# Performance work log

Hardware: AMD Instinct MI355X
Metric: run time of the kernel (lower is better)

## Reference

```python
import jax, jax.numpy as jnp
import numpy as np
from jax import lax

B, T, C, DIN, DOUT = 32, 128, 64, 32, 32  # batch, output_channels(seq), input_channels, input_dim, output_dim


def _init_params(key):
    # Mirror torch init: xOps zeros with identity on min(dout,din) diag; hOps = eye.
    # Add small noise so gradients/behavior are non-degenerate.
    k1, k2 = jax.random.split(key)
    eye_x = jnp.zeros((DOUT, DIN), jnp.float32).at[jnp.arange(min(DOUT, DIN)), jnp.arange(min(DOUT, DIN))].set(1.0)
    xOps = jnp.broadcast_to(eye_x, (4, T, C, DOUT, DIN)) + 0.02 * jax.random.normal(k1, (4, T, C, DOUT, DIN), jnp.float32)
    hOps = jnp.broadcast_to(jnp.eye(DOUT, dtype=jnp.float32), (4, T, C, DOUT, DOUT)) + 0.02 * jax.random.normal(k2, (4, T, C, DOUT, DOUT), jnp.float32)
    return xOps, hOps


def setup_inputs() -> dict:
    key = jax.random.key(0)
    kx, kp = jax.random.split(key)
    x = jax.random.normal(kx, (B, T, C, DIN), jnp.float32)
    xOps, hOps = _init_params(kp)
    return {"x": x, "xOps": xOps, "hOps": hOps}


def reference(x, xOps, hOps):
    # x: [B,T,C,Din]; xOps: [4,T,C,Dout,Din]; hOps: [4,T,C,Dout,Dout]
    b, t, c, _ = x.shape
    dout = hOps.shape[-1]
    h0 = jnp.zeros((b, c, dout), x.dtype)
    c0 = jnp.zeros((b, c, dout), x.dtype)

    def step(carry, inp):
        h, cc = carry
        x_t, xop_t, hop_t = inp  # [B,C,Din], [4,C,Dout,Din], [4,C,Dout,Dout]
        # per-channel (grouped) gate pre-activations, 4 gates at once
        X = jnp.einsum('gcij,bcj->gbci', xop_t, x_t) + jnp.einsum('gcij,bcj->gbci', hop_t, h)
        i = jax.nn.sigmoid(X[0])
        f = jax.nn.sigmoid(X[1])
        g = jnp.tanh(X[2])
        o = jax.nn.sigmoid(X[3])
        c_new = f * cc + i * g
        h_new = o * jnp.tanh(c_new)
        return (h_new, c_new), None

    xs = (jnp.swapaxes(x, 0, 1), jnp.swapaxes(xOps, 0, 1), jnp.swapaxes(hOps, 0, 1))
    (h_fin, _), _ = lax.scan(step, (h0, c0), xs)
    return h_fin  # [B,C,Dout]
```

## Files before the change

### kernel.cpp

```cpp
#include <hip/hip_runtime.h>
#include <stdint.h>

#define T_STEPS 128
#define C_CH    64
#define D_IN    32
#define D_OUT   32

#define RS 72

using frag_ab = __attribute__((ext_vector_type(8))) short;
using frag_cd = __attribute__((ext_vector_type(4))) float;

__device__ __forceinline__ void lds_barrier() {
  asm volatile("s_waitcnt lgkmcnt(0)\n\ts_barrier" ::: "memory");
}

__device__ __forceinline__ uint32_t pack_hi16(uint32_t u0, uint32_t u1) {
  return __builtin_amdgcn_perm(u1, u0, 0x07060302u);
}

__device__ __forceinline__ float fast_sigmoid(float v) {
  return __builtin_amdgcn_rcpf(1.0f + __expf(-v));
}
__device__ __forceinline__ float fast_tanh(float v) {
  return fmaf(2.0f, __builtin_amdgcn_rcpf(1.0f + __expf(-2.0f * v)), -1.0f);
}

__global__ void __launch_bounds__(256)
lstm_kernel(const float* __restrict__ x, const float* __restrict__ xOps,
            const float* __restrict__ hOps, float* __restrict__ out) {
  __shared__ short Ahi[128 * RS];
  __shared__ short Alo[128 * RS];
  __shared__ short Bhi[16 * RS];
  __shared__ short Blo[16 * RS];
  __shared__ float exch[4 * 32 * 9];

  const int tid = threadIdx.x;
  const int c   = blockIdx.x & 63;
  const int q   = blockIdx.x >> 6;

  for (int idx = tid; idx < (16 * RS) / 2; idx += 256) {
    ((uint32_t*)Bhi)[idx] = 0u;
    ((uint32_t*)Blo)[idx] = 0u;
  }

  const float* wptr[8];
  int wlds[8];
#pragma unroll
  for (int it = 0; it < 8; ++it) {
    int f  = (it * 256 + tid) * 4;
    int fh = f & 4095;
    int g  = fh >> 10;
    int i  = (fh >> 5) & 31;
    int j  = fh & 31;
    const float* base = (f < 4096) ? xOps : hOps;
    wptr[it] = base + (size_t)g * (T_STEPS * C_CH * 1024) + (size_t)c * 1024 + i * 32 + j;
    int k = j + ((f < 4096) ? 0 : 32);
    wlds[it] = (g * 32 + i) * RS + k;
  }

  const float* xptr = x;
  int xlds = 0;
  if (tid < 128) {
    int bl = tid >> 4;
    int kp = (tid & 15) * 2;
    int bg = q * 8 + bl;
    xptr = x + (size_t)bg * (T_STEPS * C_CH * D_IN) + (size_t)c * D_IN + kp;
    xlds = bl * RS + kp;
  }

  const int wave   = tid >> 6;
  const int lane   = tid & 63;
  const int frag_n = lane & 15;
  const int quad   = lane >> 4;

  const int eb = tid >> 5;
  const int ei = tid & 31;

  float4 wv[8];
#pragma unroll
  for (int it = 0; it < 8; ++it) wv[it] = *(const float4*)wptr[it];
  float2 xv = make_float2(0.f, 0.f);
  if (tid < 128) xv = *(const float2*)xptr;

  lds_barrier();

  float c_state = 0.0f;

#pragma unroll 1
  for (int t = 0; t < T_STEPS; ++t) {
#pragma unroll
    for (int it = 0; it < 8; ++it) {
      float4 v = wv[it];
      uint32_t u0 = __float_as_uint(v.x), u1 = __float_as_uint(v.y);
      uint32_t u2 = __float_as_uint(v.z), u3 = __float_as_uint(v.w);
      float r0 = v.x - __uint_as_float(u0 & 0xFFFF0000u);
      float r1 = v.y - __uint_as_float(u1 & 0xFFFF0000u);
      float r2 = v.z - __uint_as_float(u2 & 0xFFFF0000u);
      float r3 = v.w - __uint_as_float(u3 & 0xFFFF0000u);
      int s = wlds[it];
      *(uint2*)&Ahi[s] = make_uint2(pack_hi16(u0, u1), pack_hi16(u2, u3));
      *(uint2*)&Alo[s] = make_uint2(pack_hi16(__float_as_uint(r0), __float_as_uint(r1)),
                                    pack_hi16(__float_as_uint(r2), __float_as_uint(r3)));
    }
    if (tid < 128) {
      uint32_t u0 = __float_as_uint(xv.x), u1 = __float_as_uint(xv.y);
      float r0 = xv.x - __uint_as_float(u0 & 0xFFFF0000u);
      float r1 = xv.y - __uint_as_float(u1 & 0xFFFF0000u);
      *(uint32_t*)&Bhi[xlds] = pack_hi16(u0, u1);
      *(uint32_t*)&Blo[xlds] = pack_hi16(__float_as_uint(r0), __float_as_uint(r1));
    }

    if (t + 1 < T_STEPS) {
#pragma unroll
      for (int it = 0; it < 8; ++it)
        wv[it] = *(const float4*)(wptr[it] + (size_t)(t + 1) * (C_CH * 1024));
      if (tid < 128) xv = *(const float2*)(xptr + (size_t)(t + 1) * (C_CH * D_IN));
    }

    lds_barrier();

    frag_cd acc0 = {0.f, 0.f, 0.f, 0.f};
    frag_cd acc1 = {0.f, 0.f, 0.f, 0.f};
#pragma unroll
    for (int kt = 0; kt < 2; ++kt) {
      const int kk = kt * 32 + quad * 8;
      frag_ab bh = *(const frag_ab*)&Bhi[frag_n * RS + kk];
      frag_ab bl = *(const frag_ab*)&Blo[frag_n * RS + kk];
      {
        int m = wave * 32 + frag_n;
        frag_ab ah = *(const frag_ab*)&Ahi[m * RS + kk];
        frag_ab al = *(const frag_ab*)&Alo[m * RS + kk];
        acc0 = __builtin_amdgcn_mfma_f32_16x16x32_bf16(ah, bh, acc0, 0, 0, 0);
        acc0 = __builtin_amdgcn_mfma_f32_16x16x32_bf16(ah, bl, acc0, 0, 0, 0);
        acc0 = __builtin_amdgcn_mfma_f32_16x16x32_bf16(al, bh, acc0, 0, 0, 0);
      }
      {
        int m = wave * 32 + 16 + frag_n;
        frag_ab ah = *(const frag_ab*)&Ahi[m * RS + kk];
        frag_ab al = *(const frag_ab*)&Alo[m * RS + kk];
        acc1 = __builtin_amdgcn_mfma_f32_16x16x32_bf16(ah, bh, acc1, 0, 0, 0);
        acc1 = __builtin_amdgcn_mfma_f32_16x16x32_bf16(ah, bl, acc1, 0, 0, 0);
        acc1 = __builtin_amdgcn_mfma_f32_16x16x32_bf16(al, bh, acc1, 0, 0, 0);
      }
    }

    if (frag_n < 8) {
#pragma unroll
      for (int r = 0; r < 4; ++r) {
        exch[(wave * 32 + quad * 4 + r) * 9 + frag_n]      = acc0[r];
        exch[(wave * 32 + 16 + quad * 4 + r) * 9 + frag_n] = acc1[r];
      }
    }

    lds_barrier();

    {
      float X0 = exch[(0 * 32 + ei) * 9 + eb];
      float X1 = exch[(1 * 32 + ei) * 9 + eb];
      float X2 = exch[(2 * 32 + ei) * 9 + eb];
      float X3 = exch[(3 * 32 + ei) * 9 + eb];
      float ig = fast_sigmoid(X0);
      float fg = fast_sigmoid(X1);
      float gg = fast_tanh(X2);
      float og = fast_sigmoid(X3);
      c_state = fg * c_state + ig * gg;
      float hval = og * fast_tanh(c_state);
      if (t == T_STEPS - 1) {
        out[((size_t)(q * 8 + eb) * C_CH + c) * D_OUT + ei] = hval;
      } else {
        uint32_t u  = __float_as_uint(hval);
        float    r  = hval - __uint_as_float(u & 0xFFFF0000u);
        uint32_t ru = __float_as_uint(r);
        uint32_t pu  = __shfl_xor(u, 1, 64);
        uint32_t pru = __shfl_xor(ru, 1, 64);
        if ((ei & 1) == 0) {
          *(uint32_t*)&Bhi[eb * RS + 32 + ei] = pack_hi16(u, pu);
          *(uint32_t*)&Blo[eb * RS + 32 + ei] = pack_hi16(ru, pru);
        }
      }
    }
  }
}

extern "C" void kernel_launch(void* const* d_in, const int* in_sizes, int n_in,
                              void* d_out, int out_size, void* d_ws, size_t ws_size,
                              hipStream_t stream) {
  const float* x    = (const float*)d_in[0];
  const float* xOps = (const float*)d_in[1];
  const float* hOps = (const float*)d_in[2];
  lstm_kernel<<<dim3(256), dim3(256), 0, stream>>>(x, xOps, hOps, (float*)d_out);
}
```

Before: 359.2 us.

## Process all batches per channel in one block with double-buffered weight prefetch

Changes the decomposition from 256 blocks (channel × batch-quarter of 8 rows) to 64 blocks of 512 threads, each handling all 32 batch rows for one channel. Each step's weights are now read once per channel instead of four times, and loads are double-buffered two steps ahead to hide global latency. The cost is only 64 blocks on a GPU with many more CUs, so parallelism drops, and each block does more MFMA and gate work per step on the serial critical path.

```diff
diff --git a/kernel.cpp b/kernel.cpp
--- a/kernel.cpp
+++ b/kernel.cpp
@@ -7,6 +7,7 @@
 #define D_OUT   32
 
 #define RS 72
+#define ES 34
 
 using frag_ab = __attribute__((ext_vector_type(8))) short;
 using frag_cd = __attribute__((ext_vector_type(4))) float;
@@ -26,71 +27,62 @@
   return fmaf(2.0f, __builtin_amdgcn_rcpf(1.0f + __expf(-2.0f * v)), -1.0f);
 }
 
-__global__ void __launch_bounds__(256)
+__global__ void __launch_bounds__(512, 2)
 lstm_kernel(const float* __restrict__ x, const float* __restrict__ xOps,
             const float* __restrict__ hOps, float* __restrict__ out) {
   __shared__ short Ahi[128 * RS];
   __shared__ short Alo[128 * RS];
-  __shared__ short Bhi[16 * RS];
-  __shared__ short Blo[16 * RS];
-  __shared__ float exch[4 * 32 * 9];
+  __shared__ short Bhi[32 * RS];
+  __shared__ short Blo[32 * RS];
+  __shared__ float exch[4 * 32 * ES];
 
   const int tid = threadIdx.x;
-  const int c   = blockIdx.x & 63;
-  const int q   = blockIdx.x >> 6;
+  const int c   = blockIdx.x;
 
-  for (int idx = tid; idx < (16 * RS) / 2; idx += 256) {
+  for (int idx = tid; idx < (32 * RS) / 2; idx += 512) {
     ((uint32_t*)Bhi)[idx] = 0u;
     ((uint32_t*)Blo)[idx] = 0u;
   }
 
-  const float* wptr[8];
-  int wlds[8];
+  const float* wptr[4];
+  int wlds[4];
 #pragma unroll
-  for (int it = 0; it < 8; ++it) {
-    int f  = (it * 256 + tid) * 4;
+  for (int it = 0; it < 4; ++it) {
+    int f  = (it * 512 + tid) * 4;
     int fh = f & 4095;
     int g  = fh >> 10;
     int i  = (fh >> 5) & 31;
     int j  = fh & 31;
     const float* base = (f < 4096) ? xOps : hOps;
     wptr[it] = base + (size_t)g * (T_STEPS * C_CH * 1024) + (size_t)c * 1024 + i * 32 + j;
-    int k = j + ((f < 4096) ? 0 : 32);
-    wlds[it] = (g * 32 + i) * RS + k;
+    wlds[it] = (g * 32 + i) * RS + j + ((f < 4096) ? 0 : 32);
   }
 
-  const float* xptr = x;
-  int xlds = 0;
-  if (tid < 128) {
-    int bl = tid >> 4;
-    int kp = (tid & 15) * 2;
-    int bg = q * 8 + bl;
-    xptr = x + (size_t)bg * (T_STEPS * C_CH * D_IN) + (size_t)c * D_IN + kp;
-    xlds = bl * RS + kp;
-  }
+  const int bl = tid >> 4;
+  const int kp = (tid & 15) * 2;
+  const float* xptr = x + (size_t)bl * (T_STEPS * C_CH * D_IN) + (size_t)c * D_IN + kp;
+  const int xlds = bl * RS + kp;
 
-  const int wave   = tid >> 6;
-  const int lane   = tid & 63;
-  const int frag_n = lane & 15;
-  const int quad   = lane >> 4;
+  const int wave = tid >> 6;
+  const int lane = tid & 63;
+  const int g    = wave & 3;
+  const int bh   = wave >> 2;
+  const int fn   = lane & 15;
+  const int quad = lane >> 4;
 
-  const int eb = tid >> 5;
-  const int ei = tid & 31;
+  const int ei  = tid & 31;
+  const int eb0 = tid >> 5;
 
-  float4 wv[8];
+  auto load = [&](float4 wv[4], float2& xv, int t) {
 #pragma unroll
-  for (int it = 0; it < 8; ++it) wv[it] = *(const float4*)wptr[it];
-  float2 xv = make_float2(0.f, 0.f);
-  if (tid < 128) xv = *(const float2*)xptr;
+    for (int it = 0; it < 4; ++it)
+      wv[it] = *(const float4*)(wptr[it] + (size_t)t * (C_CH * 1024));
+    xv = *(const float2*)(xptr + (size_t)t * (C_CH * D_IN));
+  };
 
-  lds_barrier();
-
-  float c_state = 0.0f;
-
-#pragma unroll 1
-  for (int t = 0; t < T_STEPS; ++t) {
+  auto stage = [&](const float4 wv[4], float2 xv) {
 #pragma unroll
-    for (int it = 0; it < 8; ++it) {
+    for (int it = 0; it < 4; ++it) {
       float4 v = wv[it];
       uint32_t u0 = __float_as_uint(v.x), u1 = __float_as_uint(v.y);
       uint32_t u2 = __float_as_uint(v.z), u3 = __float_as_uint(v.w);
@@ -103,19 +95,30 @@
       *(uint2*)&Alo[s] = make_uint2(pack_hi16(__float_as_uint(r0), __float_as_uint(r1)),
                                     pack_hi16(__float_as_uint(r2), __float_as_uint(r3)));
     }
-    if (tid < 128) {
-      uint32_t u0 = __float_as_uint(xv.x), u1 = __float_as_uint(xv.y);
-      float r0 = xv.x - __uint_as_float(u0 & 0xFFFF0000u);
-      float r1 = xv.y - __uint_as_float(u1 & 0xFFFF0000u);
-      *(uint32_t*)&Bhi[xlds] = pack_hi16(u0, u1);
-      *(uint32_t*)&Blo[xlds] = pack_hi16(__float_as_uint(r0), __float_as_uint(r1));
-    }
+    uint32_t u0 = __float_as_uint(xv.x), u1 = __float_as_uint(xv.y);
+    float r0 = xv.x - __uint_as_float(u0 & 0xFFFF0000u);
+    float r1 = xv.y - __uint_as_float(u1 & 0xFFFF0000u);
+    *(uint32_t*)&Bhi[xlds] = pack_hi16(u0, u1);
+    *(uint32_t*)&Blo[xlds] = pack_hi16(__float_as_uint(r0), __float_as_uint(r1));
+  };
 
-    if (t + 1 < T_STEPS) {
-#pragma unroll
-      for (int it = 0; it < 8; ++it)
-        wv[it] = *(const float4*)(wptr[it] + (size_t)(t + 1) * (C_CH * 1024));
-      if (tid < 128) xv = *(const float2*)(xptr + (size_t)(t + 1) * (C_CH * D_IN));
+  float4 wv0[4], wv1[4];
+  float2 xv0, xv1;
+  load(wv0, xv0, 0);
+  load(wv1, xv1, 1);
+
+  lds_barrier();
+
+  float cs0 = 0.0f, cs1 = 0.0f;
+
+#pragma unroll 1
+  for (int t = 0; t < T_STEPS; ++t) {
+    if ((t & 1) == 0) {
+      stage(wv0, xv0);
+      if (t + 2 < T_STEPS) load(wv0, xv0, t + 2);
+    } else {
+      stage(wv1, xv1);
+      if (t + 2 < T_STEPS) load(wv1, xv1, t + 2);
     }
 
     lds_barrier();
@@ -125,58 +128,59 @@
 #pragma unroll
     for (int kt = 0; kt < 2; ++kt) {
       const int kk = kt * 32 + quad * 8;
-      frag_ab bh = *(const frag_ab*)&Bhi[frag_n * RS + kk];
-      frag_ab bl = *(const frag_ab*)&Blo[frag_n * RS + kk];
+      frag_ab bhf = *(const frag_ab*)&Bhi[(bh * 16 + fn) * RS + kk];
+      frag_ab blf = *(const frag_ab*)&Blo[(bh * 16 + fn) * RS + kk];
       {
-        int m = wave * 32 + frag_n;
+        int m = g * 32 + fn;
         frag_ab ah = *(const frag_ab*)&Ahi[m * RS + kk];
         frag_ab al = *(const frag_ab*)&Alo[m * RS + kk];
-        acc0 = __builtin_amdgcn_mfma_f32_16x16x32_bf16(ah, bh, acc0, 0, 0, 0);
-        acc0 = __builtin_amdgcn_mfma_f32_16x16x32_bf16(ah, bl, acc0, 0, 0, 0);
-        acc0 = __builtin_amdgcn_mfma_f32_16x16x32_bf16(al, bh, acc0, 0, 0, 0);
+        acc0 = __builtin_amdgcn_mfma_f32_16x16x32_bf16(ah, bhf, acc0, 0, 0, 0);
+        acc0 = __builtin_amdgcn_mfma_f32_16x16x32_bf16(ah, blf, acc0, 0, 0, 0);
+        acc0 = __builtin_amdgcn_mfma_f32_16x16x32_bf16(al, bhf, acc0, 0, 0, 0);
       }
       {
-        int m = wave * 32 + 16 + frag_n;
+        int m = g * 32 + 16 + fn;
         frag_ab ah = *(const frag_ab*)&Ahi[m * RS + kk];
         frag_ab al = *(const frag_ab*)&Alo[m * RS + kk];
-        acc1 = __builtin_amdgcn_mfma_f32_16x16x32_bf16(ah, bh, acc1, 0, 0, 0);
-        acc1 = __builtin_amdgcn_mfma_f32_16x16x32_bf16(ah, bl, acc1, 0, 0, 0);
-        acc1 = __builtin_amdgcn_mfma_f32_16x16x32_bf16(al, bh, acc1, 0, 0, 0);
+        acc1 = __builtin_amdgcn_mfma_f32_16x16x32_bf16(ah, bhf, acc1, 0, 0, 0);
+        acc1 = __builtin_amdgcn_mfma_f32_16x16x32_bf16(ah, blf, acc1, 0, 0, 0);
+        acc1 = __builtin_amdgcn_mfma_f32_16x16x32_bf16(al, bhf, acc1, 0, 0, 0);
       }
     }
 
-    if (frag_n < 8) {
 #pragma unroll
-      for (int r = 0; r < 4; ++r) {
-        exch[(wave * 32 + quad * 4 + r) * 9 + frag_n]      = acc0[r];
-        exch[(wave * 32 + 16 + quad * 4 + r) * 9 + frag_n] = acc1[r];
-      }
+    for (int r = 0; r < 4; ++r) {
+      exch[(g * 32 + quad * 4 + r) * ES + bh * 16 + fn]      = acc0[r];
+      exch[(g * 32 + 16 + quad * 4 + r) * ES + bh * 16 + fn] = acc1[r];
     }
 
     lds_barrier();
 
-    {
-      float X0 = exch[(0 * 32 + ei) * 9 + eb];
-      float X1 = exch[(1 * 32 + ei) * 9 + eb];
-      float X2 = exch[(2 * 32 + ei) * 9 + eb];
-      float X3 = exch[(3 * 32 + ei) * 9 + eb];
+#pragma unroll
+    for (int half = 0; half < 2; ++half) {
+      const int b = eb0 + half * 16;
+      float X0 = exch[(0 * 32 + ei) * ES + b];
+      float X1 = exch[(1 * 32 + ei) * ES + b];
+      float X2 = exch[(2 * 32 + ei) * ES + b];
+      float X3 = exch[(3 * 32 + ei) * ES + b];
       float ig = fast_sigmoid(X0);
       float fg = fast_sigmoid(X1);
       float gg = fast_tanh(X2);
       float og = fast_sigmoid(X3);
-      c_state = fg * c_state + ig * gg;
-      float hval = og * fast_tanh(c_state);
+      float& cs = half ? cs1 : cs0;
+      cs = fg * cs + ig * gg;
+      float hval = og * fast_tanh(cs);
       if (t == T_STEPS - 1) {
-        out[((size_t)(q * 8 + eb) * C_CH + c) * D_OUT + ei] = hval;
+        out[((size_t)b * C_CH + c) * D_OUT + ei] = hval;
       } else {
-        uint32_t u  = __float_as_uint(hval);
-        float    r  = hval - __uint_as_float(u & 0xFFFF0000u);
-        uint32_t ru = __float_as_uint(r);
+        uint32_t u   = __float_as_uint(hval);
+        float    rr  = hval - __uint_as_float(u & 0xFFFF0000u);
+        uint32_t ru  = __float_as_uint(rr);
         uint32_t pu  = __shfl_xor(u, 1, 64);
         uint32_t pru = __shfl_xor(ru, 1, 64);
         if ((ei & 1) == 0) {
-          *(uint32_t*)&Bhi[eb * RS + 32 + ei] = pack_hi16(u, pu);
-          *(uint32_t*)&Blo[eb * RS + 32 + ei] = pack_hi16(ru, pru);
+          *(uint32_t*)&Bhi[b * RS + 32 + ei] = pack_hi16(u, pu);
+          *(uint32_t*)&Blo[b * RS + 32 + ei] = pack_hi16(ru, pru);
         }
       }
     }
@@ -189,5 +193,5 @@
   const float* x    = (const float*)d_in[0];
   const float* xOps = (const float*)d_in[1];
   const float* hOps = (const float*)d_in[2];
-  lstm_kernel<<<dim3(256), dim3(256), 0, stream>>>(x, xOps, hOps, (float*)d_out);
+  lstm_kernel<<<dim3(C_CH), dim3(512), 0, stream>>>(x, xOps, hOps, (float*)d_out);
 }
```

New measurement: 496.7 us. +38.3%, slower.

## Replace split-bf16 MFMA gate GEMM with register-resident fp32 FMA and shuffle reduction

Applied to the files above, without the earlier changes.

Each block no longer splits weights into hi/lo bf16 halves, stages them in LDS and runs three MFMAs per tile. Each thread now keeps its slice of the weight rows in registers and does fp32 FMAs against the shared x/h vector. Partial sums across the four k-quarters are reduced with lane shuffles. Weight loads are double-buffered two steps ahead, using two register sets and an unrolled pair of steps. This removes the per-step bf16 conversion and the large LDS writes, and keeps exact fp32 accuracy, at the cost of more VALU FMAs and higher register pressure.

```diff
diff --git a/kernel.cpp b/kernel.cpp
--- a/kernel.cpp
+++ b/kernel.cpp
@@ -3,20 +3,11 @@
 
 #define T_STEPS 128
 #define C_CH    64
-#define D_IN    32
-#define D_OUT   32
-
-#define RS 72
-
-using frag_ab = __attribute__((ext_vector_type(8))) short;
-using frag_cd = __attribute__((ext_vector_type(4))) float;
+#define SROW    72
+#define EROW    10
 
 __device__ __forceinline__ void lds_barrier() {
   asm volatile("s_waitcnt lgkmcnt(0)\n\ts_barrier" ::: "memory");
-}
-
-__device__ __forceinline__ uint32_t pack_hi16(uint32_t u0, uint32_t u1) {
-  return __builtin_amdgcn_perm(u1, u0, 0x07060302u);
 }
 
 __device__ __forceinline__ float fast_sigmoid(float v) {
@@ -26,160 +17,116 @@
   return fmaf(2.0f, __builtin_amdgcn_rcpf(1.0f + __expf(-2.0f * v)), -1.0f);
 }
 
-__global__ void __launch_bounds__(256)
+__global__ void __launch_bounds__(256, 1)
 lstm_kernel(const float* __restrict__ x, const float* __restrict__ xOps,
             const float* __restrict__ hOps, float* __restrict__ out) {
-  __shared__ short Ahi[128 * RS];
-  __shared__ short Alo[128 * RS];
-  __shared__ short Bhi[16 * RS];
-  __shared__ short Blo[16 * RS];
-  __shared__ float exch[4 * 32 * 9];
+  __shared__ float S[8 * SROW];
+  __shared__ float exch[128 * EROW];
 
   const int tid = threadIdx.x;
   const int c   = blockIdx.x & 63;
   const int q   = blockIdx.x >> 6;
 
-  for (int idx = tid; idx < (16 * RS) / 2; idx += 256) {
-    ((uint32_t*)Bhi)[idx] = 0u;
-    ((uint32_t*)Blo)[idx] = 0u;
-  }
+  const int kq = tid & 3;
+  const int iq = (tid >> 2) & 15;
+  const int g  = tid >> 6;
 
-  const float* wptr[8];
-  int wlds[8];
-#pragma unroll
-  for (int it = 0; it < 8; ++it) {
-    int f  = (it * 256 + tid) * 4;
-    int fh = f & 4095;
-    int g  = fh >> 10;
-    int i  = (fh >> 5) & 31;
-    int j  = fh & 31;
-    const float* base = (f < 4096) ? xOps : hOps;
-    wptr[it] = base + (size_t)g * (T_STEPS * C_CH * 1024) + (size_t)c * 1024 + i * 32 + j;
-    int k = j + ((f < 4096) ? 0 : 32);
-    wlds[it] = (g * 32 + i) * RS + k;
-  }
+  S[(tid >> 5) * SROW + 32 + (tid & 31)] = 0.0f;
 
-  const float* xptr = x;
-  int xlds = 0;
-  if (tid < 128) {
-    int bl = tid >> 4;
-    int kp = (tid & 15) * 2;
-    int bg = q * 8 + bl;
-    xptr = x + (size_t)bg * (T_STEPS * C_CH * D_IN) + (size_t)c * D_IN + kp;
-    xlds = bl * RS + kp;
-  }
+  const float* wbase = (kq < 2) ? xOps : hOps;
+  const int    jo    = (kq & 1) * 16;
+  const float* wp0 = wbase + ((size_t)g * T_STEPS * C_CH + c) * 1024 + iq * 32 + jo;
+  const float* wp1 = wp0 + 512;
+  const size_t WT  = (size_t)C_CH * 1024;
 
-  const int wave   = tid >> 6;
-  const int lane   = tid & 63;
-  const int frag_n = lane & 15;
-  const int quad   = lane >> 4;
+  const int bx = tid >> 3, jx = (tid & 7) * 4;
+  const float* xp = x + (size_t)(q * 8 + bx) * (T_STEPS * C_CH * 32) + c * 32 + jx;
+  const size_t XT = (size_t)C_CH * 32;
 
   const int eb = tid >> 5;
   const int ei = tid & 31;
 
-  float4 wv[8];
+  auto loadw = [&](float4 w0[4], float4 w1[4], int t) {
 #pragma unroll
-  for (int it = 0; it < 8; ++it) wv[it] = *(const float4*)wptr[it];
-  float2 xv = make_float2(0.f, 0.f);
-  if (tid < 128) xv = *(const float2*)xptr;
+    for (int it = 0; it < 4; ++it) {
+      w0[it] = *(const float4*)(wp0 + (size_t)t * WT + it * 4);
+      w1[it] = *(const float4*)(wp1 + (size_t)t * WT + it * 4);
+    }
+  };
 
-  lds_barrier();
+  float4 wa0[4], wa1[4], wb0[4], wb1[4];
+  float4 xa = make_float4(0.f, 0.f, 0.f, 0.f), xb = xa;
+  loadw(wa0, wa1, 0);
+  loadw(wb0, wb1, 1);
+  if (tid < 64) { xa = *(const float4*)xp; xb = *(const float4*)(xp + XT); }
 
-  float c_state = 0.0f;
+  float cs = 0.0f;
 
-#pragma unroll 1
-  for (int t = 0; t < T_STEPS; ++t) {
-#pragma unroll
-    for (int it = 0; it < 8; ++it) {
-      float4 v = wv[it];
-      uint32_t u0 = __float_as_uint(v.x), u1 = __float_as_uint(v.y);
-      uint32_t u2 = __float_as_uint(v.z), u3 = __float_as_uint(v.w);
-      float r0 = v.x - __uint_as_float(u0 & 0xFFFF0000u);
-      float r1 = v.y - __uint_as_float(u1 & 0xFFFF0000u);
-      float r2 = v.z - __uint_as_float(u2 & 0xFFFF0000u);
-      float r3 = v.w - __uint_as_float(u3 & 0xFFFF0000u);
-      int s = wlds[it];
-      *(uint2*)&Ahi[s] = make_uint2(pack_hi16(u0, u1), pack_hi16(u2, u3));
-      *(uint2*)&Alo[s] = make_uint2(pack_hi16(__float_as_uint(r0), __float_as_uint(r1)),
-                                    pack_hi16(__float_as_uint(r2), __float_as_uint(r3)));
-    }
-    if (tid < 128) {
-      uint32_t u0 = __float_as_uint(xv.x), u1 = __float_as_uint(xv.y);
-      float r0 = xv.x - __uint_as_float(u0 & 0xFFFF0000u);
-      float r1 = xv.y - __uint_as_float(u1 & 0xFFFF0000u);
-      *(uint32_t*)&Bhi[xlds] = pack_hi16(u0, u1);
-      *(uint32_t*)&Blo[xlds] = pack_hi16(__float_as_uint(r0), __float_as_uint(r1));
-    }
-
-    if (t + 1 < T_STEPS) {
-#pragma unroll
-      for (int it = 0; it < 8; ++it)
-        wv[it] = *(const float4*)(wptr[it] + (size_t)(t + 1) * (C_CH * 1024));
-      if (tid < 128) xv = *(const float2*)(xptr + (size_t)(t + 1) * (C_CH * D_IN));
-    }
-
+  auto step = [&](int t, float4 w0[4], float4 w1[4], float4& xv) {
+    if (tid < 64) *(float4*)&S[bx * SROW + jx] = xv;
     lds_barrier();
 
-    frag_cd acc0 = {0.f, 0.f, 0.f, 0.f};
-    frag_cd acc1 = {0.f, 0.f, 0.f, 0.f};
+    float acc0[8], acc1[8];
 #pragma unroll
-    for (int kt = 0; kt < 2; ++kt) {
-      const int kk = kt * 32 + quad * 8;
-      frag_ab bh = *(const frag_ab*)&Bhi[frag_n * RS + kk];
-      frag_ab bl = *(const frag_ab*)&Blo[frag_n * RS + kk];
-      {
-        int m = wave * 32 + frag_n;
-        frag_ab ah = *(const frag_ab*)&Ahi[m * RS + kk];
-        frag_ab al = *(const frag_ab*)&Alo[m * RS + kk];
-        acc0 = __builtin_amdgcn_mfma_f32_16x16x32_bf16(ah, bh, acc0, 0, 0, 0);
-        acc0 = __builtin_amdgcn_mfma_f32_16x16x32_bf16(ah, bl, acc0, 0, 0, 0);
-        acc0 = __builtin_amdgcn_mfma_f32_16x16x32_bf16(al, bh, acc0, 0, 0, 0);
-      }
-      {
-        int m = wave * 32 + 16 + frag_n;
-        frag_ab ah = *(const frag_ab*)&Ahi[m * RS + kk];
-        frag_ab al = *(const frag_ab*)&Alo[m * RS + kk];
-        acc1 = __builtin_amdgcn_mfma_f32_16x16x32_bf16(ah, bh, acc1, 0, 0, 0);
-        acc1 = __builtin_amdgcn_mfma_f32_16x16x32_bf16(ah, bl, acc1, 0, 0, 0);
-        acc1 = __builtin_amdgcn_mfma_f32_16x16x32_bf16(al, bh, acc1, 0, 0, 0);
+    for (int b = 0; b < 8; ++b) { acc0[b] = 0.f; acc1[b] = 0.f; }
+#pragma unroll
+    for (int it = 0; it < 4; ++it) {
+#pragma unroll
+      for (int b = 0; b < 8; ++b) {
+        float4 sv = *(const float4*)&S[b * SROW + kq * 16 + it * 4];
+        acc0[b] = fmaf(w0[it].x, sv.x, acc0[b]);
+        acc0[b] = fmaf(w0[it].y, sv.y, acc0[b]);
+        acc0[b] = fmaf(w0[it].z, sv.z, acc0[b]);
+        acc0[b] = fmaf(w0[it].w, sv.w, acc0[b]);
+        acc1[b] = fmaf(w1[it].x, sv.x, acc1[b]);
+        acc1[b] = fmaf(w1[it].y, sv.y, acc1[b]);
+        acc1[b] = fmaf(w1[it].z, sv.z, acc1[b]);
+        acc1[b] = fmaf(w1[it].w, sv.w, acc1[b]);
       }
     }
 
-    if (frag_n < 8) {
-#pragma unroll
-      for (int r = 0; r < 4; ++r) {
-        exch[(wave * 32 + quad * 4 + r) * 9 + frag_n]      = acc0[r];
-        exch[(wave * 32 + 16 + quad * 4 + r) * 9 + frag_n] = acc1[r];
-      }
+    if (t + 2 < T_STEPS) {
+      loadw(w0, w1, t + 2);
+      if (tid < 64) xv = *(const float4*)(xp + (size_t)(t + 2) * XT);
     }
 
+#pragma unroll
+    for (int b = 0; b < 8; ++b) {
+      acc0[b] += __shfl_xor(acc0[b], 1, 64);
+      acc0[b] += __shfl_xor(acc0[b], 2, 64);
+      acc1[b] += __shfl_xor(acc1[b], 1, 64);
+      acc1[b] += __shfl_xor(acc1[b], 2, 64);
+    }
+    {
+      const int b0 = kq * 2;
+      *(float2*)&exch[(g * 32 + iq) * EROW + b0]      = make_float2(acc0[b0], acc0[b0 + 1]);
+      *(float2*)&exch[(g * 32 + 16 + iq) * EROW + b0] = make_float2(acc1[b0], acc1[b0 + 1]);
+    }
     lds_barrier();
 
     {
-      float X0 = exch[(0 * 32 + ei) * 9 + eb];
-      float X1 = exch[(1 * 32 + ei) * 9 + eb];
-      float X2 = exch[(2 * 32 + ei) * 9 + eb];
-      float X3 = exch[(3 * 32 + ei) * 9 + eb];
+      float X0 = exch[(0 * 32 + ei) * EROW + eb];
+      float X1 = exch[(1 * 32 + ei) * EROW + eb];
+      float X2 = exch[(2 * 32 + ei) * EROW + eb];
+      float X3 = exch[(3 * 32 + ei) * EROW + eb];
       float ig = fast_sigmoid(X0);
       float fg = fast_sigmoid(X1);
       float gg = fast_tanh(X2);
       float og = fast_sigmoid(X3);
-      c_state = fg * c_state + ig * gg;
-      float hval = og * fast_tanh(c_state);
+      cs = fg * cs + ig * gg;
+      float hval = og * fast_tanh(cs);
       if (t == T_STEPS - 1) {
-        out[((size_t)(q * 8 + eb) * C_CH + c) * D_OUT + ei] = hval;
+        out[((size_t)(q * 8 + eb) * C_CH + c) * 32 + ei] = hval;
       } else {
-        uint32_t u  = __float_as_uint(hval);
-        float    r  = hval - __uint_as_float(u & 0xFFFF0000u);
-        uint32_t ru = __float_as_uint(r);
-        uint32_t pu  = __shfl_xor(u, 1, 64);
-        uint32_t pru = __shfl_xor(ru, 1, 64);
-        if ((ei & 1) == 0) {
-          *(uint32_t*)&Bhi[eb * RS + 32 + ei] = pack_hi16(u, pu);
-          *(uint32_t*)&Blo[eb * RS + 32 + ei] = pack_hi16(ru, pru);
-        }
+        S[eb * SROW + 32 + ei] = hval;
       }
     }
+  };
+
+#pragma unroll 1
+  for (int t = 0; t < T_STEPS; t += 2) {
+    step(t,     wa0, wa1, xa);
+    step(t + 1, wb0, wb1, xb);
   }
 }
 
```

Result: slower. 501.7 us (+39.7%).
